# Kernel tuning notes

Hardware: AMD Instinct MI355X
Metric: run time of the kernel (lower is better)

The kernel has to match this reference:

```python
import jax, jax.numpy as jnp
import numpy as np
from jax.ops import segment_sum

NUM_NODES = 50000
IN_DIM = 512
OUT_DIM = 512
NNZ = 150000
NUM_EDGES = 10000


def setup_inputs() -> dict:
    key = jax.random.key(0)
    k1, k2, k3, k4, k5 = jax.random.split(key, 5)
    X = jax.random.normal(k1, (NUM_NODES, IN_DIM), dtype=jnp.float32)
    V = jax.random.randint(k2, (NNZ,), 0, NUM_NODES)
    E = jax.random.randint(k3, (NNZ,), 0, NUM_EDGES)
    # Linear(in_dim, out_dim) params (torch default init ~ U(-1/sqrt(in), 1/sqrt(in)))
    bound = 1.0 / np.sqrt(IN_DIM)
    W = jax.random.uniform(k4, (OUT_DIM, IN_DIM), minval=-bound, maxval=bound, dtype=jnp.float32)
    b = jax.random.uniform(k5, (OUT_DIM,), minval=-bound, maxval=bound, dtype=jnp.float32)
    eps = jnp.float32(0.1)
    return {"X": X, "V": V, "E": E, "num_edges": NUM_EDGES, "W": W, "b": b, "eps": eps}


def reference(X, V, E, num_edges, W, b, eps):
    num_nodes = X.shape[0]
    # Stage 1: node -> hyperedge (mean of member node features)
    gathered = X[V]  # (nnz, in_dim)
    edge_sum = segment_sum(gathered, E, num_segments=num_edges)          # (num_edges, in_dim)
    count = segment_sum(jnp.ones((E.shape[0],), X.dtype), E, num_segments=num_edges)
    edge_emb = edge_sum / jnp.clip(count, 1.0)[:, None]
    # Stage 2: hyperedge -> node (sum of incident hyperedge embeddings)
    node_msg = segment_sum(edge_emb[E], V, num_segments=num_nodes)       # (num_nodes, in_dim)
    # GIN self-loop + linear
    h = (1.0 + eps) * X + node_msg
    return h @ W.T + b
```

## Files before the change

kernel.cpp:

```cpp
#include <hip/hip_runtime.h>

#define D     512
#define NEDGE 10000
#define ECAP  64
#define NCAP  32
#define CPAD  32

typedef __attribute__((ext_vector_type(8))) short  bf16x8;
typedef __attribute__((ext_vector_type(4))) float  f32x4;
typedef __attribute__((ext_vector_type(8))) unsigned short u16x8;

static __device__ __forceinline__ unsigned short f2bf(float f) {
    union { float f; unsigned u; } c; c.f = f;
    unsigned u = c.u;
    return (unsigned short)((u + 0x7FFFu + ((u >> 16) & 1u)) >> 16);
}
static __device__ __forceinline__ float bf2f(unsigned short s) {
    union { unsigned u; float f; } c; c.u = ((unsigned)s) << 16; return c.f;
}

__global__ __launch_bounds__(256)
void adj_build(const int* __restrict__ V, const int* __restrict__ E,
               const float* __restrict__ W,
               int* __restrict__ ecnt, int* __restrict__ ncnt,
               int* __restrict__ emem, int* __restrict__ nmem,
               unsigned short* __restrict__ wb, int nnz)
{
    const int i = blockIdx.x * 256 + threadIdx.x;
    if (i < nnz) {
        const int e = E[i], v = V[i];
        const int p = atomicAdd(&ecnt[(size_t)e * CPAD], 1);
        if (p < ECAP) emem[e * ECAP + p] = v;
        const int q = atomicAdd(&ncnt[(size_t)v * CPAD], 1);
        if (q < NCAP) nmem[v * NCAP + q] = e;
    }
    if (i < D * D / 8) {
        const float4 a = *(reinterpret_cast<const float4*>(W) + (size_t)i * 2);
        const float4 b = *(reinterpret_cast<const float4*>(W) + (size_t)i * 2 + 1);
        u16x8 o;
        o[0] = f2bf(a.x); o[1] = f2bf(a.y); o[2] = f2bf(a.z); o[3] = f2bf(a.w);
        o[4] = f2bf(b.x); o[5] = f2bf(b.y); o[6] = f2bf(b.z); o[7] = f2bf(b.w);
        *(reinterpret_cast<u16x8*>(wb) + i) = o;
    }
}

__global__ __launch_bounds__(256)
void edge_gather(const float* __restrict__ X, const int* __restrict__ ecnt,
                 const int* __restrict__ emem, unsigned short* __restrict__ edge_emb)
{
    __shared__ float red[D];
    const int e = blockIdx.x;
    const int t = threadIdx.x;
    const int half = t >> 7;
    const int l = t & 127;
    int deg = ecnt[(size_t)e * CPAD]; if (deg > ECAP) deg = ECAP;
    const int* lst = emem + e * ECAP;
    float4 acc = make_float4(0.f, 0.f, 0.f, 0.f);
    for (int m = half; m < deg; m += 2) {
        const int v = lst[m];
        const float4 x = *reinterpret_cast<const float4*>(X + (size_t)v * D + l * 4);
        acc.x += x.x; acc.y += x.y; acc.z += x.z; acc.w += x.w;
    }
    if (half) *reinterpret_cast<float4*>(red + l * 4) = acc;
    __syncthreads();
    if (!half) {
        const float4 o = *reinterpret_cast<const float4*>(red + l * 4);
        const float inv = 1.0f / fmaxf((float)deg, 1.0f);
        ushort4 r;
        r.x = f2bf((acc.x + o.x) * inv);
        r.y = f2bf((acc.y + o.y) * inv);
        r.z = f2bf((acc.z + o.z) * inv);
        r.w = f2bf((acc.w + o.w) * inv);
        *reinterpret_cast<ushort4*>(edge_emb + (size_t)e * D + l * 4) = r;
    }
}

__global__ __launch_bounds__(128)
void build_h(const float* __restrict__ X, const unsigned short* __restrict__ edge_emb,
             const int* __restrict__ ncnt, const int* __restrict__ nmem,
             const float* __restrict__ eps_p, unsigned short* __restrict__ h, int M)
{
    const int v = blockIdx.x;
    const int t = threadIdx.x;
    float4 acc = make_float4(0.f, 0.f, 0.f, 0.f);
    if (v < M) {
        const float scale = 1.0f + *eps_p;
        const float4 x = *reinterpret_cast<const float4*>(X + (size_t)v * D + t * 4);
        acc.x = scale * x.x; acc.y = scale * x.y;
        acc.z = scale * x.z; acc.w = scale * x.w;
        int deg = ncnt[(size_t)v * CPAD]; if (deg > NCAP) deg = NCAP;
        const int* lst = nmem + v * NCAP;
        for (int m = 0; m < deg; ++m) {
            const int e = lst[m];
            const ushort4 g = *reinterpret_cast<const ushort4*>(edge_emb + (size_t)e * D + t * 4);
            acc.x += bf2f(g.x); acc.y += bf2f(g.y);
            acc.z += bf2f(g.z); acc.w += bf2f(g.w);
        }
    }
    ushort4 r;
    r.x = f2bf(acc.x); r.y = f2bf(acc.y); r.z = f2bf(acc.z); r.w = f2bf(acc.w);
    *reinterpret_cast<ushort4*>(h + (size_t)v * D + t * 4) = r;
}

__global__ __launch_bounds__(256, 5)
void gemm_bf16(const unsigned short* __restrict__ h, const unsigned short* __restrict__ wb,
               const float* __restrict__ bias, float* __restrict__ out, int M,
               int q, int r)
{
    __shared__ unsigned short As[128 * 64];
    __shared__ unsigned short Bs[128 * 64];

    const int orig = blockIdx.x;
    const int xcd = orig & 7, lin = orig >> 3;
    const int wg = (xcd < r ? xcd * (q + 1) : r * (q + 1) + (xcd - r) * q) + lin;
    const int row0 = (wg >> 2) * 128;
    const int col0 = (wg & 3) * 128;

    const int tid  = threadIdx.x;
    const int lane = tid & 63;
    const int wave = tid >> 6;
    const int wr = wave >> 1, wc = wave & 1;

    const int l15   = lane & 15;
    const int khalf = lane >> 4;
    const int crow  = lane >> 3;
    const int slot  = lane & 7;

    f32x4 acc[4][4] = {};

    for (int t = 0; t < 8; ++t) {
        const int k0 = t * 64;
        #pragma unroll
        for (int cc = 0; cc < 8; ++cc) {
            const int chunk = wave * 8 + cc;
            const unsigned short* src; unsigned short* dst; int c, base;
            if (chunk < 16) { c = chunk;      src = h;  base = row0; dst = As; }
            else            { c = chunk - 16; src = wb; base = col0; dst = Bs; }
            const int rr = c * 8 + crow;
            const int gslot = slot ^ (rr & 7);
            const unsigned short* gp = src + (size_t)(base + rr) * D + k0 + gslot * 8;
            unsigned short* lp = dst + c * 512;
            __builtin_amdgcn_global_load_lds(
                (const __attribute__((address_space(1))) void*)gp,
                (__attribute__((address_space(3))) void*)lp, 16, 0, 0);
        }
        asm volatile("s_waitcnt vmcnt(0)" ::: "memory");
        __syncthreads();

        #pragma unroll
        for (int s = 0; s < 2; ++s) {
            bf16x8 a[4], b[4];
            #pragma unroll
            for (int i = 0; i < 4; ++i) {
                const int rr = wr * 64 + i * 16 + l15;
                const int sl = (khalf | (s << 2)) ^ (rr & 7);
                a[i] = *reinterpret_cast<const bf16x8*>(As + rr * 64 + sl * 8);
            }
            #pragma unroll
            for (int j = 0; j < 4; ++j) {
                const int rr = wc * 64 + j * 16 + l15;
                const int sl = (khalf | (s << 2)) ^ (rr & 7);
                b[j] = *reinterpret_cast<const bf16x8*>(Bs + rr * 64 + sl * 8);
            }
            #pragma unroll
            for (int i = 0; i < 4; ++i)
                #pragma unroll
                for (int j = 0; j < 4; ++j)
                    acc[i][j] = __builtin_amdgcn_mfma_f32_16x16x32_bf16(a[i], b[j], acc[i][j], 0, 0, 0);
        }
        __syncthreads();
    }

    const int row4 = (lane >> 4) * 4;
    #pragma unroll
    for (int j = 0; j < 4; ++j) {
        const int gc = col0 + wc * 64 + j * 16 + l15;
        const float bv = bias[gc];
        #pragma unroll
        for (int i = 0; i < 4; ++i) {
            #pragma unroll
            for (int reg = 0; reg < 4; ++reg) {
                const int gr = row0 + wr * 64 + i * 16 + row4 + reg;
                if (gr < M) out[(size_t)gr * D + gc] = acc[i][j][reg] + bv;
            }
        }
    }
}

extern "C" void kernel_launch(void* const* d_in, const int* in_sizes, int n_in,
                              void* d_out, int out_size, void* d_ws, size_t ws_size,
                              hipStream_t stream)
{
    const float* X    = (const float*)d_in[0];
    const int*   V    = (const int*)  d_in[1];
    const int*   E    = (const int*)  d_in[2];
    const float* W    = (const float*)d_in[4];
    const float* bias = (const float*)d_in[5];
    const float* eps  = (const float*)d_in[6];
    float* out = (float*)d_out;

    const int nnz = in_sizes[1];
    const int M   = in_sizes[0] / D;
    const int Mpad = ((M + 127) / 128) * 128;

    char* w = (char*)d_ws;
    int* ecnt = (int*)w;
    int* ncnt = ecnt + (size_t)NEDGE * CPAD;
    size_t off = ((size_t)NEDGE + Mpad) * CPAD * sizeof(int);
    int* emem = (int*)(w + off);            off += (size_t)NEDGE * ECAP * sizeof(int);
    int* nmem = (int*)(w + off);            off += (size_t)M * NCAP * sizeof(int);
    off = (off + 255) & ~(size_t)255;
    unsigned short* edge_emb = (unsigned short*)(w + off); off += (size_t)NEDGE * D * sizeof(unsigned short);
    unsigned short* hbuf     = (unsigned short*)(w + off); off += (size_t)Mpad * D * sizeof(unsigned short);
    unsigned short* wbuf     = (unsigned short*)(w + off); off += (size_t)D * D * sizeof(unsigned short);

    hipMemsetAsync(ecnt, 0, ((size_t)NEDGE + Mpad) * CPAD * sizeof(int), stream);

    adj_build<<<(nnz + 255) / 256, 256, 0, stream>>>(V, E, W, ecnt, ncnt, emem, nmem,
                                                     wbuf, nnz);
    edge_gather<<<NEDGE, 256, 0, stream>>>(X, ecnt, emem, edge_emb);
    build_h    <<<Mpad, 128, 0, stream>>>(X, edge_emb, ncnt, nmem, eps, hbuf, M);

    const int nwg = (Mpad / 128) * (D / 128);
    gemm_bf16<<<nwg, 256, 0, stream>>>(hbuf, wbuf, bias, out, M, nwg / 8, nwg % 8);
}
```

Measured before the change: 168.7 us.

## Apply linear layer before aggregation so gathers move bf16 projected features

```diff
diff --git a/kernel.cpp b/kernel.cpp
--- a/kernel.cpp
+++ b/kernel.cpp
@@ -44,9 +44,111 @@
     }
 }
 
+__global__ __launch_bounds__(256, 5)
+void gemm_xw(const float* __restrict__ X, const unsigned short* __restrict__ wb,
+             unsigned short* __restrict__ y, int M, int q, int r)
+{
+    __shared__ unsigned short As[128 * 64];
+    __shared__ unsigned short Bs[128 * 64];
+
+    const int orig = blockIdx.x;
+    const int xcd = orig & 7, lin = orig >> 3;
+    const int wg = (xcd < r ? xcd * (q + 1) : r * (q + 1) + (xcd - r) * q) + lin;
+    const int row0 = (wg >> 2) * 128;
+    const int col0 = (wg & 3) * 128;
+
+    const int tid  = threadIdx.x;
+    const int lane = tid & 63;
+    const int wave = tid >> 6;
+    const int wr = wave >> 1, wc = wave & 1;
+
+    const int l15   = lane & 15;
+    const int khalf = lane >> 4;
+    const int crow  = lane >> 3;
+    const int slot  = lane & 7;
+
+    const int arow  = tid >> 1;
+    const int ahalf = tid & 1;
+    const int gr0   = row0 + arow;
+    const float* xrow = X + (size_t)(gr0 < M ? gr0 : M - 1) * D + ahalf * 32;
+    unsigned short* awr = As + arow * 64;
+    const int aswz = arow & 7;
+
+    f32x4 acc[4][4] = {};
+
+    for (int t = 0; t < 8; ++t) {
+        const int k0 = t * 64;
+        #pragma unroll
+        for (int cc = 0; cc < 4; ++cc) {
+            const int c = wave * 4 + cc;
+            const int rr = c * 8 + crow;
+            const int gslot = slot ^ (rr & 7);
+            const unsigned short* gp = wb + (size_t)(col0 + rr) * D + k0 + gslot * 8;
+            unsigned short* lp = Bs + c * 512;
+            __builtin_amdgcn_global_load_lds(
+                (const __attribute__((address_space(1))) void*)gp,
+                (__attribute__((address_space(3))) void*)lp, 16, 0, 0);
+        }
+        #pragma unroll
+        for (int u = 0; u < 4; ++u) {
+            const float4 a  = *reinterpret_cast<const float4*>(xrow + k0 + u * 8);
+            const float4 b2 = *reinterpret_cast<const float4*>(xrow + k0 + u * 8 + 4);
+            u16x8 o;
+            o[0] = f2bf(a.x);  o[1] = f2bf(a.y);  o[2] = f2bf(a.z);  o[3] = f2bf(a.w);
+            o[4] = f2bf(b2.x); o[5] = f2bf(b2.y); o[6] = f2bf(b2.z); o[7] = f2bf(b2.w);
+            const int s = ahalf * 4 + u;
+            *reinterpret_cast<u16x8*>(awr + (s ^ aswz) * 8) = o;
+        }
+        asm volatile("s_waitcnt vmcnt(0)" ::: "memory");
+        __syncthreads();
+
+        #pragma unroll
+        for (int s = 0; s < 2; ++s) {
+            bf16x8 a[4], b[4];
+            #pragma unroll
+            for (int i = 0; i < 4; ++i) {
+                const int rr = wr * 64 + i * 16 + l15;
+                const int sl = (khalf | (s << 2)) ^ (rr & 7);
+                a[i] = *reinterpret_cast<const bf16x8*>(As + rr * 64 + sl * 8);
+            }
+            #pragma unroll
+            for (int j = 0; j < 4; ++j) {
+                const int rr = wc * 64 + j * 16 + l15;
+                const int sl = (khalf | (s << 2)) ^ (rr & 7);
+                b[j] = *reinterpret_cast<const bf16x8*>(Bs + rr * 64 + sl * 8);
+            }
+            #pragma unroll
+            for (int i = 0; i < 4; ++i)
+                #pragma unroll
+                for (int j = 0; j < 4; ++j)
+                    acc[i][j] = __builtin_amdgcn_mfma_f32_16x16x32_bf16(a[i], b[j], acc[i][j], 0, 0, 0);
+        }
+        __syncthreads();
+    }
+
+    const int row4 = (lane >> 4) * 4;
+    #pragma unroll
+    for (int j = 0; j < 4; ++j) {
+        const int gc = col0 + wc * 64 + j * 16 + l15;
+        #pragma unroll
+        for (int i = 0; i < 4; ++i) {
+            #pragma unroll
+            for (int reg = 0; reg < 4; ++reg) {
+                const int gr = row0 + wr * 64 + i * 16 + row4 + reg;
+                const float own = acc[i][j][reg];
+                const float nb  = __shfl_xor(own, 1);
+                if (!(lane & 1)) {
+                    const unsigned dw = (unsigned)f2bf(own) | ((unsigned)f2bf(nb) << 16);
+                    *reinterpret_cast<unsigned*>(y + (size_t)gr * D + gc) = dw;
+                }
+            }
+        }
+    }
+}
+
 __global__ __launch_bounds__(256)
-void edge_gather(const float* __restrict__ X, const int* __restrict__ ecnt,
-                 const int* __restrict__ emem, unsigned short* __restrict__ edge_emb)
+void edge_gather(const unsigned short* __restrict__ y, const int* __restrict__ ecnt,
+                 const int* __restrict__ emem, unsigned short* __restrict__ ey)
 {
     __shared__ float red[D];
     const int e = blockIdx.x;
@@ -58,8 +160,9 @@
     float4 acc = make_float4(0.f, 0.f, 0.f, 0.f);
     for (int m = half; m < deg; m += 2) {
         const int v = lst[m];
-        const float4 x = *reinterpret_cast<const float4*>(X + (size_t)v * D + l * 4);
-        acc.x += x.x; acc.y += x.y; acc.z += x.z; acc.w += x.w;
+        const ushort4 x = *reinterpret_cast<const ushort4*>(y + (size_t)v * D + l * 4);
+        acc.x += bf2f(x.x); acc.y += bf2f(x.y);
+        acc.z += bf2f(x.z); acc.w += bf2f(x.w);
     }
     if (half) *reinterpret_cast<float4*>(red + l * 4) = acc;
     __syncthreads();
@@ -71,120 +174,36 @@
         r.y = f2bf((acc.y + o.y) * inv);
         r.z = f2bf((acc.z + o.z) * inv);
         r.w = f2bf((acc.w + o.w) * inv);
-        *reinterpret_cast<ushort4*>(edge_emb + (size_t)e * D + l * 4) = r;
+        *reinterpret_cast<ushort4*>(ey + (size_t)e * D + l * 4) = r;
     }
 }
 
 __global__ __launch_bounds__(128)
-void build_h(const float* __restrict__ X, const unsigned short* __restrict__ edge_emb,
-             const int* __restrict__ ncnt, const int* __restrict__ nmem,
-             const float* __restrict__ eps_p, unsigned short* __restrict__ h, int M)
+void build_out(const unsigned short* __restrict__ y, const unsigned short* __restrict__ ey,
+               const int* __restrict__ ncnt, const int* __restrict__ nmem,
+               const float* __restrict__ eps_p, const float* __restrict__ bias,
+               float* __restrict__ out, int M)
 {
     const int v = blockIdx.x;
+    if (v >= M) return;
     const int t = threadIdx.x;
-    float4 acc = make_float4(0.f, 0.f, 0.f, 0.f);
-    if (v < M) {
-        const float scale = 1.0f + *eps_p;
-        const float4 x = *reinterpret_cast<const float4*>(X + (size_t)v * D + t * 4);
-        acc.x = scale * x.x; acc.y = scale * x.y;
-        acc.z = scale * x.z; acc.w = scale * x.w;
-        int deg = ncnt[(size_t)v * CPAD]; if (deg > NCAP) deg = NCAP;
-        const int* lst = nmem + v * NCAP;
-        for (int m = 0; m < deg; ++m) {
-            const int e = lst[m];
-            const ushort4 g = *reinterpret_cast<const ushort4*>(edge_emb + (size_t)e * D + t * 4);
-            acc.x += bf2f(g.x); acc.y += bf2f(g.y);
-            acc.z += bf2f(g.z); acc.w += bf2f(g.w);
-        }
-    }
-    ushort4 r;
-    r.x = f2bf(acc.x); r.y = f2bf(acc.y); r.z = f2bf(acc.z); r.w = f2bf(acc.w);
-    *reinterpret_cast<ushort4*>(h + (size_t)v * D + t * 4) = r;
-}
-
-__global__ __launch_bounds__(256, 5)
-void gemm_bf16(const unsigned short* __restrict__ h, const unsigned short* __restrict__ wb,
-               const float* __restrict__ bias, float* __restrict__ out, int M,
-               int q, int r)
-{
-    __shared__ unsigned short As[128 * 64];
-    __shared__ unsigned short Bs[128 * 64];
-
-    const int orig = blockIdx.x;
-    const int xcd = orig & 7, lin = orig >> 3;
-    const int wg = (xcd < r ? xcd * (q + 1) : r * (q + 1) + (xcd - r) * q) + lin;
-    const int row0 = (wg >> 2) * 128;
-    const int col0 = (wg & 3) * 128;
-
-    const int tid  = threadIdx.x;
-    const int lane = tid & 63;
-    const int wave = tid >> 6;
-    const int wr = wave >> 1, wc = wave & 1;
-
-    const int l15   = lane & 15;
-    const int khalf = lane >> 4;
-    const int crow  = lane >> 3;
-    const int slot  = lane & 7;
-
-    f32x4 acc[4][4] = {};
-
-    for (int t = 0; t < 8; ++t) {
-        const int k0 = t * 64;
-        #pragma unroll
-        for (int cc = 0; cc < 8; ++cc) {
-            const int chunk = wave * 8 + cc;
-            const unsigned short* src; unsigned short* dst; int c, base;
-            if (chunk < 16) { c = chunk;      src = h;  base = row0; dst = As; }
-            else            { c = chunk - 16; src = wb; base = col0; dst = Bs; }
-            const int rr = c * 8 + crow;
-            const int gslot = slot ^ (rr & 7);
-            const unsigned short* gp = src + (size_t)(base + rr) * D + k0 + gslot * 8;
-            unsigned short* lp = dst + c * 512;
-            __builtin_amdgcn_global_load_lds(
-                (const __attribute__((address_space(1))) void*)gp,
-                (__attribute__((address_space(3))) void*)lp, 16, 0, 0);
-        }
-        asm volatile("s_waitcnt vmcnt(0)" ::: "memory");
-        __syncthreads();
-
-        #pragma unroll
-        for (int s = 0; s < 2; ++s) {
-            bf16x8 a[4], b[4];
-            #pragma unroll
-            for (int i = 0; i < 4; ++i) {
-                const int rr = wr * 64 + i * 16 + l15;
-                const int sl = (khalf | (s << 2)) ^ (rr & 7);
-                a[i] = *reinterpret_cast<const bf16x8*>(As + rr * 64 + sl * 8);
-            }
-            #pragma unroll
-            for (int j = 0; j < 4; ++j) {
-                const int rr = wc * 64 + j * 16 + l15;
-                const int sl = (khalf | (s << 2)) ^ (rr & 7);
-                b[j] = *reinterpret_cast<const bf16x8*>(Bs + rr * 64 + sl * 8);
-            }
-            #pragma unroll
-            for (int i = 0; i < 4; ++i)
-                #pragma unroll
-                for (int j = 0; j < 4; ++j)
-                    acc[i][j] = __builtin_amdgcn_mfma_f32_16x16x32_bf16(a[i], b[j], acc[i][j], 0, 0, 0);
-        }
-        __syncthreads();
-    }
-
-    const int row4 = (lane >> 4) * 4;
-    #pragma unroll
-    for (int j = 0; j < 4; ++j) {
-        const int gc = col0 + wc * 64 + j * 16 + l15;
-        const float bv = bias[gc];
-        #pragma unroll
-        for (int i = 0; i < 4; ++i) {
-            #pragma unroll
-            for (int reg = 0; reg < 4; ++reg) {
-                const int gr = row0 + wr * 64 + i * 16 + row4 + reg;
-                if (gr < M) out[(size_t)gr * D + gc] = acc[i][j][reg] + bv;
-            }
-        }
-    }
+    const float scale = 1.0f + *eps_p;
+    const ushort4 yv = *reinterpret_cast<const ushort4*>(y + (size_t)v * D + t * 4);
+    const float4 bv = *reinterpret_cast<const float4*>(bias + t * 4);
+    float4 acc;
+    acc.x = scale * bf2f(yv.x) + bv.x;
+    acc.y = scale * bf2f(yv.y) + bv.y;
+    acc.z = scale * bf2f(yv.z) + bv.z;
+    acc.w = scale * bf2f(yv.w) + bv.w;
+    int deg = ncnt[(size_t)v * CPAD]; if (deg > NCAP) deg = NCAP;
+    const int* lst = nmem + v * NCAP;
+    for (int m = 0; m < deg; ++m) {
+        const int e = lst[m];
+        const ushort4 g = *reinterpret_cast<const ushort4*>(ey + (size_t)e * D + t * 4);
+        acc.x += bf2f(g.x); acc.y += bf2f(g.y);
+        acc.z += bf2f(g.z); acc.w += bf2f(g.w);
+    }
+    *reinterpret_cast<float4*>(out + (size_t)v * D + t * 4) = acc;
 }
 
 extern "C" void kernel_launch(void* const* d_in, const int* in_sizes, int n_in,
@@ -210,17 +229,18 @@
     int* emem = (int*)(w + off);            off += (size_t)NEDGE * ECAP * sizeof(int);
     int* nmem = (int*)(w + off);            off += (size_t)M * NCAP * sizeof(int);
     off = (off + 255) & ~(size_t)255;
-    unsigned short* edge_emb = (unsigned short*)(w + off); off += (size_t)NEDGE * D * sizeof(unsigned short);
-    unsigned short* hbuf     = (unsigned short*)(w + off); off += (size_t)Mpad * D * sizeof(unsigned short);
-    unsigned short* wbuf     = (unsigned short*)(w + off); off += (size_t)D * D * sizeof(unsigned short);
+    unsigned short* ybuf = (unsigned short*)(w + off); off += (size_t)Mpad * D * sizeof(unsigned short);
+    unsigned short* eybf = (unsigned short*)(w + off); off += (size_t)NEDGE * D * sizeof(unsigned short);
+    unsigned short* wbuf = (unsigned short*)(w + off); off += (size_t)D * D * sizeof(unsigned short);
 
     hipMemsetAsync(ecnt, 0, ((size_t)NEDGE + Mpad) * CPAD * sizeof(int), stream);
 
     adj_build<<<(nnz + 255) / 256, 256, 0, stream>>>(V, E, W, ecnt, ncnt, emem, nmem,
                                                      wbuf, nnz);
-    edge_gather<<<NEDGE, 256, 0, stream>>>(X, ecnt, emem, edge_emb);
-    build_h    <<<Mpad, 128, 0, stream>>>(X, edge_emb, ncnt, nmem, eps, hbuf, M);
 
     const int nwg = (Mpad / 128) * (D / 128);
-    gemm_bf16<<<nwg, 256, 0, stream>>>(hbuf, wbuf, bias, out, M, nwg / 8, nwg % 8);
-}
+    gemm_xw<<<nwg, 256, 0, stream>>>(X, wbuf, ybuf, M, nwg / 8, nwg % 8);
+
+    edge_gather<<<NEDGE, 256, 0, stream>>>(ybuf, ecnt, emem, eybf);
+    build_out  <<<M, 128, 0, stream>>>(ybuf, eybf, ncnt, nmem, eps, bias, out, M);
+}
```

Measured after the change: 344.1 us. 2.04x slower.
